# Kernel tuning notes

Hardware: AMD Instinct MI355X
Metric: run time of the kernel (lower is better)

Reference implementation:

```python
import jax, jax.numpy as jnp
import numpy as np

NUM_NODES = 100000
NUM_RELS = 50
NUM_BASES = 16
H_DIM = 16
OUT_DIM = 8
NUM_EDGES = 3200000


def setup_inputs() -> dict:
    key = jax.random.key(0)
    ks = jax.random.split(key, 10)
    inp = {
        "edge_src": jax.random.randint(ks[0], (NUM_EDGES,), 0, NUM_NODES, dtype=jnp.int32),
        "edge_dst": jax.random.randint(ks[1], (NUM_EDGES,), 0, NUM_NODES, dtype=jnp.int32),
        "edge_type": jax.random.randint(ks[2], (NUM_EDGES,), 0, NUM_RELS, dtype=jnp.int32),
        "edge_norm": jax.random.uniform(ks[3], (NUM_EDGES,), dtype=jnp.float32),
        "W0": jax.random.normal(ks[4], (NUM_BASES, NUM_NODES, H_DIM), dtype=jnp.float32) * 0.05,
        "C0": jax.random.normal(ks[5], (NUM_RELS, NUM_BASES), dtype=jnp.float32) * 0.05,
        "W1": jax.random.normal(ks[6], (NUM_BASES, H_DIM, H_DIM), dtype=jnp.float32) * 0.05,
        "C1": jax.random.normal(ks[7], (NUM_RELS, NUM_BASES), dtype=jnp.float32) * 0.05,
        "W2": jax.random.normal(ks[8], (NUM_BASES, H_DIM, OUT_DIM), dtype=jnp.float32) * 0.05,
        "C2": jax.random.normal(ks[9], (NUM_RELS, NUM_BASES), dtype=jnp.float32) * 0.05,
    }
    return inp


def _input_layer(src, dst, rel, norm, W0, C0):
    # basis combination: (R, N, h) embedding-per-relation table
    Wfull = jnp.einsum('rb,bnh->rnh', C0, W0)
    emb = Wfull.reshape(NUM_RELS * NUM_NODES, H_DIM)
    # per-edge gather by rel_type * in_feat + src_id, scaled by norm
    msg = emb[rel * NUM_NODES + src] * norm[:, None]
    h = jax.ops.segment_sum(msg, dst, num_segments=NUM_NODES)
    return jax.nn.relu(h)


def _dense_layer(h, src, dst, rel, norm, W, C, out_dim):
    # basis combination: (R, in, out)
    Wr = jnp.einsum('rb,bio->rio', C, W)
    # transform node features once per relation, then gather by (rel, src)
    Hr = jnp.einsum('ni,rio->rno', h, Wr)  # (R, N, out)
    msg = Hr[rel, src] * norm[:, None]     # (E, out)
    return jax.ops.segment_sum(msg, dst, num_segments=NUM_NODES)


def reference(edge_src, edge_dst, edge_type, edge_norm, W0, C0, W1, C1, W2, C2):
    h = _input_layer(edge_src, edge_dst, edge_type, edge_norm, W0, C0)
    h = jax.nn.relu(_dense_layer(h, edge_src, edge_dst, edge_type, edge_norm, W1, C1, H_DIM))
    h = jax.nn.softmax(_dense_layer(h, edge_src, edge_dst, edge_type, edge_norm, W2, C2, OUT_DIM), axis=1)
    return h
```

## Files before the change

kernel.cpp:

```cpp
#include <hip/hip_runtime.h>
#include <cstddef>
#include <cstdint>

#define E_TOTAL 3200000
#define N_NODES 100000
#define N_RELS 50
#define N_BASES 16
#define HD 16
#define OD 8
#define NTHR 256

#define NBKT 196
#define P1B 1024
#define P1C 3125
#define FP8_SCALE 256.0f
#define FP8_INV (1.0f / 256.0f)

typedef unsigned int u32;
typedef __attribute__((ext_vector_type(8))) short s16x8;
typedef __attribute__((ext_vector_type(4))) float f32x4;
typedef __attribute__((ext_vector_type(16))) float f32x16;

__device__ __forceinline__ u32 cvtpk(float x0, float x1) {
    u32 r;
    asm("v_cvt_pk_bf16_f32 %0, %1, %2" : "=v"(r) : "v"(x0), "v"(x1));
    return r;
}
__device__ __forceinline__ ushort bf16r(float x) {
    u32 a = __float_as_uint(x);
    return (ushort)((a + 0x7fffu + ((a >> 16) & 1u)) >> 16);
}
__device__ __forceinline__ s16x8 as_s16x8(uint4 u) {
    union { uint4 u; s16x8 s; } x; x.u = u; return x.s;
}

#if __has_builtin(__builtin_amdgcn_cvt_pk_fp8_f32)
__device__ __forceinline__ u32 pk8x4(float a, float b, float c, float d) {
    int v = __builtin_amdgcn_cvt_pk_fp8_f32(a, b, 0, false);
    v = __builtin_amdgcn_cvt_pk_fp8_f32(c, d, v, true);
    return (u32)v;
}
#else
__device__ __forceinline__ u32 pk8(float v) {
    u32 x = __float_as_uint(v);
    u32 s = (x >> 24) & 0x80u;
    u32 ax = x & 0x7fffffffu;
    int e = (int)(ax >> 23) - 127;
    if (e < -9) return s;
    if (e < -6) {
        u32 m = (u32)rintf(__uint_as_float(ax) * 512.0f);
        if (m == 0) return s;
        if (m >= 8) return s | 0x08u;
        return s | m;
    }
    u32 m = ax & 0x7fffffu;
    u32 keep = m >> 20, rest = m & 0xFFFFFu;
    keep += (rest > 0x80000u) || (rest == 0x80000u && (keep & 1u));
    u32 ee = (u32)(e + 7);
    if (keep == 8u) { keep = 0u; ee += 1u; }
    if (ee > 15u || (ee == 15u && keep == 7u)) return s | 0x7eu;
    return s | (ee << 3) | keep;
}
__device__ __forceinline__ u32 pk8x4(float a, float b, float c, float d) {
    return pk8(a) | (pk8(b) << 8) | (pk8(c) << 16) | (pk8(d) << 24);
}
#endif
#if __has_builtin(__builtin_amdgcn_cvt_f32_fp8)
template <int SEL>
__device__ __forceinline__ float up8(u32 q) { return __builtin_amdgcn_cvt_f32_fp8(q, SEL); }
#else
template <int SEL>
__device__ __forceinline__ float up8(u32 q) {
    u32 b = (q >> (SEL * 8)) & 0xffu;
    u32 em = b & 0x7fu;
    float v = (em >= 8u) ? __uint_as_float((((em >> 3) + 120u) << 23) | ((em & 7u) << 20))
                         : (float)em * (1.0f / 512.0f);
    return (b & 0x80u) ? -v : v;
}
#endif

__global__ __launch_bounds__(NTHR) void k_p1(const int* __restrict__ esrc, const int* __restrict__ edst,
                                             const int* __restrict__ erel, const float* __restrict__ enorm,
                                             uint2* __restrict__ tmp, int* __restrict__ cntK,
                                             int* __restrict__ runstartK,
                                             const float* __restrict__ W1, const float* __restrict__ C1,
                                             const float* __restrict__ W2, const float* __restrict__ C2,
                                             ushort* __restrict__ f1, ushort* __restrict__ f2) {
    __shared__ int lcnt[NBKT];
    __shared__ int sc[NTHR];
    __shared__ int lcur[NBKT];
    __shared__ uint2 stage[P1C];
    int tid = threadIdx.x;
    if (blockIdx.x >= P1B) {
        int idx = (blockIdx.x - P1B) * NTHR + tid;
        if (idx < 25 * 512) {
            int p = idx >> 9, rem = idx & 511, lane = rem >> 3, e = rem & 7;
            int m = lane & 31, kk = ((lane >> 5) << 3) + e;
            int r = 2 * p + (m >> 4), o = m & 15;
            float acc = 0.f;
            #pragma unroll
            for (int b = 0; b < N_BASES; ++b)
                acc = fmaf(C1[r * N_BASES + b], W1[b * 256 + kk * 16 + o], acc);
            f1[idx] = bf16r(acc * FP8_SCALE);
        } else if (idx < 25 * 512 + 13 * 512) {
            int j = idx - 25 * 512;
            int g = j >> 9, rem = j & 511, lane = rem >> 3, e = rem & 7;
            int m = lane & 31, kk = ((lane >> 5) << 3) + e;
            int rl = 4 * g + (m >> 3), o = m & 7;
            float acc = 0.f;
            if (rl < N_RELS) {
                #pragma unroll
                for (int b = 0; b < N_BASES; ++b)
                    acc = fmaf(C2[rl * N_BASES + b], W2[b * 128 + kk * 8 + o], acc);
            }
            f2[j] = bf16r(acc * FP8_SCALE);
        }
        return;
    }
    for (int i = tid; i < NBKT; i += NTHR) lcnt[i] = 0;
    __syncthreads();
    int e0 = blockIdx.x * P1C;
    u32 rx[13], rn[13];
    int rb[13];
    #pragma unroll
    for (int j = 0; j < 13; ++j) {
        int i = tid + j * NTHR;
        rb[j] = -1;
        if (i < P1C) {
            int e = e0 + i;
            int d = edst[e];
            int b = d >> 9;
            rb[j] = b;
            rx[j] = (u32)esrc[e] | ((u32)erel[e] << 17) | ((u32)(d & 511) << 23);
            rn[j] = __float_as_uint(enorm[e]);
            atomicAdd(&lcnt[b], 1);
        }
    }
    __syncthreads();
    int own = (tid < NBKT) ? lcnt[tid] : 0;
    sc[tid] = own;
    __syncthreads();
    #pragma unroll
    for (int off = 1; off < NTHR; off <<= 1) {
        int t = (tid >= off) ? sc[tid - off] : 0;
        __syncthreads();
        sc[tid] += t;
        __syncthreads();
    }
    if (tid < NBKT) lcur[tid] = sc[tid] - own;
    __syncthreads();
    #pragma unroll
    for (int j = 0; j < 13; ++j) {
        if (rb[j] >= 0) {
            int pos = atomicAdd(&lcur[rb[j]], 1);
            stage[pos] = make_uint2(rx[j], rn[j]);
        }
    }
    __syncthreads();
    for (int i = tid; i < P1C; i += NTHR)
        tmp[(size_t)blockIdx.x * P1C + i] = stage[i];
    for (int b = tid; b < NBKT; b += NTHR) {
        int excl = lcur[b] - lcnt[b];
        cntK[blockIdx.x * NBKT + b] = lcnt[b];
        runstartK[blockIdx.x * NBKT + b] = blockIdx.x * P1C + excl;
    }
}

__global__ __launch_bounds__(NTHR) void k_tot(const int* __restrict__ cntK, int* __restrict__ total) {
    int b = blockIdx.x;
    __shared__ int s[NTHR];
    int tid = threadIdx.x;
    int acc = 0;
    for (int k = tid; k < P1B; k += NTHR) acc += cntK[k * NBKT + b];
    s[tid] = acc;
    __syncthreads();
    for (int off = NTHR / 2; off > 0; off >>= 1) {
        if (tid < off) s[tid] += s[tid + off];
        __syncthreads();
    }
    if (tid == 0) total[b] = s[0];
}

__global__ __launch_bounds__(1024) void k_p2(const uint2* __restrict__ tmp, const int* __restrict__ cntK,
                                             const int* __restrict__ runstartK, const int* __restrict__ total,
                                             uint2* __restrict__ rec, int* __restrict__ row_ptr) {
    int b = blockIdx.x;
    int tid = threadIdx.x;
    __shared__ int dcnt[512], dscan[512];
    __shared__ int gbs;
    if (tid < 256) dcnt[tid] = (tid < b && tid < NBKT) ? total[tid] : 0;
    __syncthreads();
    for (int off = 128; off > 0; off >>= 1) {
        if (tid < off) dcnt[tid] += dcnt[tid + off];
        __syncthreads();
    }
    if (tid == 0) gbs = dcnt[0];
    __syncthreads();
    int gbase = gbs;
    if (tid < 512) dcnt[tid] = 0;
    __syncthreads();
    int mycnt = cntK[tid * NBKT + b];
    int myrs = runstartK[tid * NBKT + b];
    for (int i = 0; i < mycnt; ++i)
        atomicAdd(&dcnt[tmp[myrs + i].x >> 23], 1);
    __syncthreads();
    if (tid < 512) dscan[tid] = dcnt[tid];
    __syncthreads();
    for (int off = 1; off < 512; off <<= 1) {
        int v = (tid >= off && tid < 512) ? dscan[tid - off] : 0;
        __syncthreads();
        if (tid < 512) dscan[tid] += v;
        __syncthreads();
    }
    if (tid < 512) {
        int excl = gbase + dscan[tid] - dcnt[tid];
        int d = (b << 9) + tid;
        if (d < N_NODES) row_ptr[d] = excl;
        dscan[tid] = excl;
    }
    if (b == NBKT - 1 && tid == 0) row_ptr[N_NODES] = E_TOTAL;
    __syncthreads();
    for (int i = 0; i < mycnt; ++i) {
        uint2 t = tmp[myrs + i];
        int pos = atomicAdd(&dscan[t.x >> 23], 1);
        rec[pos] = make_uint2(t.x & 0x7FFFFFu, t.y);
    }
}


__global__ __launch_bounds__(NTHR) void k_emb0(const float* __restrict__ W0, const float* __restrict__ C0,
                                               u32* __restrict__ emb) {
    int tid = threadIdx.x;
    int slot0 = (blockIdx.x * NTHR + tid) * 4;
    __shared__ float c[N_RELS * 16];
    for (int i = tid; i < N_RELS * 16; i += NTHR) c[i] = C0[i] * FP8_SCALE;
    bool ok = slot0 < N_NODES * HD;
    float w[4][16];
    if (ok) {
        #pragma unroll
        for (int b = 0; b < 16; ++b) {
            float4 v = *(const float4*)(W0 + (size_t)b * (N_NODES * HD) + slot0);
            w[0][b] = v.x; w[1][b] = v.y; w[2][b] = v.z; w[3][b] = v.w;
        }
    }
    __syncthreads();
    if (!ok) return;
    for (int r = 0; r < N_RELS; ++r) {
        const float* cr = c + r * 16;
        float a0 = 0.f, a1 = 0.f, a2 = 0.f, a3 = 0.f;
        #pragma unroll
        for (int b = 0; b < 16; ++b) {
            float cb = cr[b];
            a0 = fmaf(cb, w[0][b], a0);
            a1 = fmaf(cb, w[1][b], a1);
            a2 = fmaf(cb, w[2][b], a2);
            a3 = fmaf(cb, w[3][b], a3);
        }
        emb[r * (N_NODES * HD / 4) + (slot0 >> 2)] = pk8x4(a0, a1, a2, a3);
    }
}

__global__ __launch_bounds__(NTHR) void k_g16b(const uint2* __restrict__ rec, const int* __restrict__ row_ptr,
                                               const u32* __restrict__ tbl, u32* __restrict__ hb) {
    int lane = threadIdx.x & 63;
    int g = lane >> 2, l = lane & 3;
    int wave = (blockIdx.x * NTHR + threadIdx.x) >> 6;
    int nw = (gridDim.x * NTHR) >> 6;
    for (int d = wave; d < N_NODES; d += nw) {
        int s0 = row_ptr[d], s1 = row_ptr[d + 1];
        float a0 = 0.f, a1 = 0.f, a2 = 0.f, a3 = 0.f;
        for (int j = s0 + g; j < s1; j += 16) {
            uint2 rc = rec[j];
            int src = rc.x & 0x1FFFF;
            int rel = rc.x >> 17;
            float nm = __uint_as_float(rc.y) * FP8_INV;
            u32 q = tbl[((size_t)rel * N_NODES + src) * 4 + l];
            a0 = fmaf(nm, up8<0>(q), a0);
            a1 = fmaf(nm, up8<1>(q), a1);
            a2 = fmaf(nm, up8<2>(q), a2);
            a3 = fmaf(nm, up8<3>(q), a3);
        }
        a0 += __shfl_xor(a0, 4);  a1 += __shfl_xor(a1, 4);  a2 += __shfl_xor(a2, 4);  a3 += __shfl_xor(a3, 4);
        a0 += __shfl_xor(a0, 8);  a1 += __shfl_xor(a1, 8);  a2 += __shfl_xor(a2, 8);  a3 += __shfl_xor(a3, 8);
        a0 += __shfl_xor(a0, 16); a1 += __shfl_xor(a1, 16); a2 += __shfl_xor(a2, 16); a3 += __shfl_xor(a3, 16);
        a0 += __shfl_xor(a0, 32); a1 += __shfl_xor(a1, 32); a2 += __shfl_xor(a2, 32); a3 += __shfl_xor(a3, 32);
        if (lane < 4) {
            uint2 pk = make_uint2(cvtpk(fmaxf(a0, 0.f), fmaxf(a1, 0.f)),
                                  cvtpk(fmaxf(a2, 0.f), fmaxf(a3, 0.f)));
            *(uint2*)(hb + (size_t)d * 8 + l * 2) = pk;
        }
    }
}

__global__ __launch_bounds__(NTHR) void k_e1f(const uint4* __restrict__ wfrag, const uint4* __restrict__ hb,
                                              u32* __restrict__ emb) {
    const f32x16 z16 = {0.f, 0.f, 0.f, 0.f, 0.f, 0.f, 0.f, 0.f,
                        0.f, 0.f, 0.f, 0.f, 0.f, 0.f, 0.f, 0.f};
    int lane = threadIdx.x & 63;
    int w = (blockIdx.x * NTHR + threadIdx.x) >> 6;
    int p = w / 250, c = w % 250;
    if (p >= 25) return;
    s16x8 af = as_s16x8(wfrag[p * 64 + lane]);
    int col = lane & 31, hi = lane >> 5;
    size_t r0b = (size_t)(2 * p) * 400000, r1b = (size_t)(2 * p + 1) * 400000;
    for (int t = c; t < 3125; t += 250) {
        uint4 hq = hb[(size_t)(t * 32 + col) * 2 + hi];
        f32x16 d = __builtin_amdgcn_mfma_f32_32x32x16_bf16(af, as_s16x8(hq), z16, 0, 0, 0);
        u32 A0 = pk8x4(d[0], d[1], d[2], d[3]);
        u32 B0 = pk8x4(d[4], d[5], d[6], d[7]);
        u32 A1 = pk8x4(d[8], d[9], d[10], d[11]);
        u32 B1 = pk8x4(d[12], d[13], d[14], d[15]);
        u32 pA0 = (u32)__shfl_xor((int)A0, 32);
        u32 pB0 = (u32)__shfl_xor((int)B0, 32);
        u32 pA1 = (u32)__shfl_xor((int)A1, 32);
        u32 pB1 = (u32)__shfl_xor((int)B1, 32);
        u32 off = t * 128 + col * 4;
        if (hi == 0) {
            *(uint2*)(emb + r0b + off) = make_uint2(A0, pA0);
            *(uint2*)(emb + r1b + off) = make_uint2(A1, pA1);
        } else {
            *(uint2*)(emb + r0b + off + 2) = make_uint2(pB0, B0);
            *(uint2*)(emb + r1b + off + 2) = make_uint2(pB1, B1);
        }
    }
}

__global__ __launch_bounds__(NTHR) void k_e2f(const uint4* __restrict__ wfrag, const uint4* __restrict__ hb,
                                              u32* __restrict__ emb) {
    const f32x16 z16 = {0.f, 0.f, 0.f, 0.f, 0.f, 0.f, 0.f, 0.f,
                        0.f, 0.f, 0.f, 0.f, 0.f, 0.f, 0.f, 0.f};
    int lane = threadIdx.x & 63;
    int w = (blockIdx.x * NTHR + threadIdx.x) >> 6;
    int g = w / 250, c = w % 250;
    if (g >= 13) return;
    s16x8 af = as_s16x8(wfrag[g * 64 + lane]);
    int col = lane & 31, hi = lane >> 5;
    for (int t = c; t < 3125; t += 250) {
        uint4 hq = hb[(size_t)(t * 32 + col) * 2 + hi];
        f32x16 d = __builtin_amdgcn_mfma_f32_32x32x16_bf16(af, as_s16x8(hq), z16, 0, 0, 0);
        #pragma unroll
        for (int j = 0; j < 4; ++j) {
            int rl = 4 * g + j;
            if (rl >= N_RELS) break;
            u32 wj = pk8x4(d[4 * j], d[4 * j + 1], d[4 * j + 2], d[4 * j + 3]);
            emb[(size_t)rl * 200000 + t * 64 + col * 2 + hi] = wj;
        }
    }
}

__global__ __launch_bounds__(NTHR) void k_g8sm(const uint2* __restrict__ rec, const int* __restrict__ row_ptr,
                                               const u32* __restrict__ tbl, float* __restrict__ out) {
    int lane = threadIdx.x & 63;
    int g = lane >> 1, l = lane & 1;
    int wave = (blockIdx.x * NTHR + threadIdx.x) >> 6;
    int nw = (gridDim.x * NTHR) >> 6;
    for (int d = wave; d < N_NODES; d += nw) {
        int s0 = row_ptr[d], s1 = row_ptr[d + 1];
        float a0 = 0.f, a1 = 0.f, a2 = 0.f, a3 = 0.f;
        for (int j = s0 + g; j < s1; j += 32) {
            uint2 rc = rec[j];
            int src = rc.x & 0x1FFFF;
            int rel = rc.x >> 17;
            float nm = __uint_as_float(rc.y) * FP8_INV;
            u32 q = tbl[((size_t)rel * N_NODES + src) * 2 + l];
            a0 = fmaf(nm, up8<0>(q), a0);
            a1 = fmaf(nm, up8<1>(q), a1);
            a2 = fmaf(nm, up8<2>(q), a2);
            a3 = fmaf(nm, up8<3>(q), a3);
        }
        a0 += __shfl_xor(a0, 2);  a1 += __shfl_xor(a1, 2);  a2 += __shfl_xor(a2, 2);  a3 += __shfl_xor(a3, 2);
        a0 += __shfl_xor(a0, 4);  a1 += __shfl_xor(a1, 4);  a2 += __shfl_xor(a2, 4);  a3 += __shfl_xor(a3, 4);
        a0 += __shfl_xor(a0, 8);  a1 += __shfl_xor(a1, 8);  a2 += __shfl_xor(a2, 8);  a3 += __shfl_xor(a3, 8);
        a0 += __shfl_xor(a0, 16); a1 += __shfl_xor(a1, 16); a2 += __shfl_xor(a2, 16); a3 += __shfl_xor(a3, 16);
        a0 += __shfl_xor(a0, 32); a1 += __shfl_xor(a1, 32); a2 += __shfl_xor(a2, 32); a3 += __shfl_xor(a3, 32);
        float mx = fmaxf(fmaxf(a0, a1), fmaxf(a2, a3));
        mx = fmaxf(mx, __shfl_xor(mx, 1));
        float e0 = __expf(a0 - mx), e1 = __expf(a1 - mx), e2 = __expf(a2 - mx), e3 = __expf(a3 - mx);
        float sm = e0 + e1 + e2 + e3;
        sm += __shfl_xor(sm, 1);
        float inv = 1.0f / sm;
        if (lane < 2)
            *(float4*)(out + (size_t)d * OD + l * 4) = make_float4(e0 * inv, e1 * inv, e2 * inv, e3 * inv);
    }
}

#define NBLK 2560

__device__ __forceinline__ void fma4(float* acc, float c, float4 w) {
    acc[0] = fmaf(c, w.x, acc[0]);
    acc[1] = fmaf(c, w.y, acc[1]);
    acc[2] = fmaf(c, w.z, acc[2]);
    acc[3] = fmaf(c, w.w, acc[3]);
}

__global__ __launch_bounds__(NTHR) void k_wr(const float* __restrict__ W1, const float* __restrict__ C1,
                                             const float* __restrict__ W2, const float* __restrict__ C2,
                                             float* __restrict__ Wr1, float* __restrict__ Wr2) {
    int idx = blockIdx.x * NTHR + threadIdx.x;
    const int n1 = N_RELS * 256;
    if (idx < n1) {
        int r = idx >> 8, io = idx & 255;
        float acc = 0.f;
        #pragma unroll
        for (int b = 0; b < N_BASES; ++b)
            acc = fmaf(C1[r * N_BASES + b], W1[b * 256 + io], acc);
        Wr1[idx] = acc;
    } else if (idx < n1 + N_RELS * 128) {
        int j = idx - n1;
        int r = j >> 7, io = j & 127;
        float acc = 0.f;
        #pragma unroll
        for (int b = 0; b < N_BASES; ++b)
            acc = fmaf(C2[r * N_BASES + b], W2[b * 128 + io], acc);
        Wr2[j] = acc;
    }
}

__global__ __launch_bounds__(NTHR) void k_l0_old(const int* __restrict__ esrc, const int* __restrict__ edst,
                                                 const int* __restrict__ erel, const float* __restrict__ enorm,
                                                 const float* __restrict__ W0, const float* __restrict__ C0,
                                                 float* __restrict__ h0) {
    for (int e = blockIdx.x * NTHR + threadIdx.x; e < E_TOTAL; e += NBLK * NTHR) {
        int s = esrc[e], d = edst[e], r = erel[e];
        float nm = enorm[e];
        const float4* cp = reinterpret_cast<const float4*>(C0 + r * N_BASES);
        float4 c0 = cp[0], c1 = cp[1], c2 = cp[2], c3 = cp[3];
        float coef[16] = {c0.x, c0.y, c0.z, c0.w, c1.x, c1.y, c1.z, c1.w,
                          c2.x, c2.y, c2.z, c2.w, c3.x, c3.y, c3.z, c3.w};
        float acc[16];
        #pragma unroll
        for (int h = 0; h < 16; ++h) acc[h] = 0.f;
        const float* wbase = W0 + (size_t)s * HD;
        #pragma unroll
        for (int b = 0; b < N_BASES; ++b) {
            const float4* wp = reinterpret_cast<const float4*>(wbase + (size_t)b * (N_NODES * HD));
            float cb = coef[b];
            fma4(acc + 0, cb, wp[0]);
            fma4(acc + 4, cb, wp[1]);
            fma4(acc + 8, cb, wp[2]);
            fma4(acc + 12, cb, wp[3]);
        }
        float* outp = h0 + (size_t)d * HD;
        #pragma unroll
        for (int h = 0; h < 16; ++h) atomicAdd(outp + h, nm * acc[h]);
    }
}

__global__ __launch_bounds__(NTHR) void k_l1_old(const int* __restrict__ esrc, const int* __restrict__ edst,
                                                 const int* __restrict__ erel, const float* __restrict__ enorm,
                                                 const float* __restrict__ h0, const float* __restrict__ Wr1,
                                                 float* __restrict__ h1) {
    __shared__ float w[N_RELS * 260];
    for (int i = threadIdx.x; i < N_RELS * 256; i += NTHR) {
        int r = i >> 8, rest = i & 255;
        w[r * 260 + rest] = Wr1[i];
    }
    __syncthreads();
    for (int e = blockIdx.x * NTHR + threadIdx.x; e < E_TOTAL; e += NBLK * NTHR) {
        int s = esrc[e], d = edst[e], r = erel[e];
        float nm = enorm[e];
        const float4* hp = reinterpret_cast<const float4*>(h0 + (size_t)s * HD);
        float4 hv0 = hp[0], hv1 = hp[1], hv2 = hp[2], hv3 = hp[3];
        float hs[16] = {fmaxf(hv0.x, 0.f), fmaxf(hv0.y, 0.f), fmaxf(hv0.z, 0.f), fmaxf(hv0.w, 0.f),
                        fmaxf(hv1.x, 0.f), fmaxf(hv1.y, 0.f), fmaxf(hv1.z, 0.f), fmaxf(hv1.w, 0.f),
                        fmaxf(hv2.x, 0.f), fmaxf(hv2.y, 0.f), fmaxf(hv2.z, 0.f), fmaxf(hv2.w, 0.f),
                        fmaxf(hv3.x, 0.f), fmaxf(hv3.y, 0.f), fmaxf(hv3.z, 0.f), fmaxf(hv3.w, 0.f)};
        float acc[16];
        #pragma unroll
        for (int h = 0; h < 16; ++h) acc[h] = 0.f;
        const float* wr = w + r * 260;
        #pragma unroll
        for (int i = 0; i < 16; ++i) {
            float hi = hs[i];
            const float4* wp = reinterpret_cast<const float4*>(wr + i * 16);
            fma4(acc + 0, hi, wp[0]);
            fma4(acc + 4, hi, wp[1]);
            fma4(acc + 8, hi, wp[2]);
            fma4(acc + 12, hi, wp[3]);
        }
        float* outp = h1 + (size_t)d * HD;
        #pragma unroll
        for (int h = 0; h < 16; ++h) atomicAdd(outp + h, nm * acc[h]);
    }
}

__global__ __launch_bounds__(NTHR) void k_l2_old(const int* __restrict__ esrc, const int* __restrict__ edst,
                                                 const int* __restrict__ erel, const float* __restrict__ enorm,
                                                 const float* __restrict__ h1, const float* __restrict__ Wr2,
                                                 float* __restrict__ h2) {
    __shared__ float w[N_RELS * 132];
    for (int i = threadIdx.x; i < N_RELS * 128; i += NTHR) {
        int r = i >> 7, rest = i & 127;
        w[r * 132 + rest] = Wr2[i];
    }
    __syncthreads();
    for (int e = blockIdx.x * NTHR + threadIdx.x; e < E_TOTAL; e += NBLK * NTHR) {
        int s = esrc[e], d = edst[e], r = erel[e];
        float nm = enorm[e];
        const float4* hp = reinterpret_cast<const float4*>(h1 + (size_t)s * HD);
        float4 hv0 = hp[0], hv1 = hp[1], hv2 = hp[2], hv3 = hp[3];
        float hs[16] = {fmaxf(hv0.x, 0.f), fmaxf(hv0.y, 0.f), fmaxf(hv0.z, 0.f), fmaxf(hv0.w, 0.f),
                        fmaxf(hv1.x, 0.f), fmaxf(hv1.y, 0.f), fmaxf(hv1.z, 0.f), fmaxf(hv1.w, 0.f),
                        fmaxf(hv2.x, 0.f), fmaxf(hv2.y, 0.f), fmaxf(hv2.z, 0.f), fmaxf(hv2.w, 0.f),
                        fmaxf(hv3.x, 0.f), fmaxf(hv3.y, 0.f), fmaxf(hv3.z, 0.f), fmaxf(hv3.w, 0.f)};
        float acc[8];
        #pragma unroll
        for (int h = 0; h < 8; ++h) acc[h] = 0.f;
        const float* wr = w + r * 132;
        #pragma unroll
        for (int i = 0; i < 16; ++i) {
            float hi = hs[i];
            const float4* wp = reinterpret_cast<const float4*>(wr + i * 8);
            fma4(acc + 0, hi, wp[0]);
            fma4(acc + 4, hi, wp[1]);
        }
        float* outp = h2 + (size_t)d * OD;
        #pragma unroll
        for (int h = 0; h < 8; ++h) atomicAdd(outp + h, nm * acc[h]);
    }
}

__global__ __launch_bounds__(NTHR) void k_softmax(const float* __restrict__ h2, float* __restrict__ out) {
    int n = blockIdx.x * NTHR + threadIdx.x;
    if (n >= N_NODES) return;
    const float4* p = reinterpret_cast<const float4*>(h2 + (size_t)n * OD);
    float4 a = p[0], b = p[1];
    float v[8] = {a.x, a.y, a.z, a.w, b.x, b.y, b.z, b.w};
    float m = v[0];
    #pragma unroll
    for (int i = 1; i < 8; ++i) m = fmaxf(m, v[i]);
    float ssum = 0.f;
    #pragma unroll
    for (int i = 0; i < 8; ++i) {
        v[i] = __expf(v[i] - m);
        ssum += v[i];
    }
    float inv = 1.0f / ssum;
    float4* q = reinterpret_cast<float4*>(out + (size_t)n * OD);
    q[0] = make_float4(v[0] * inv, v[1] * inv, v[2] * inv, v[3] * inv);
    q[1] = make_float4(v[4] * inv, v[5] * inv, v[6] * inv, v[7] * inv);
}


extern "C" void kernel_launch(void* const* d_in, const int* in_sizes, int n_in,
                              void* d_out, int out_size, void* d_ws, size_t ws_size,
                              hipStream_t stream) {
    const int* esrc = (const int*)d_in[0];
    const int* edst = (const int*)d_in[1];
    const int* erel = (const int*)d_in[2];
    const float* enorm = (const float*)d_in[3];
    const float* W0 = (const float*)d_in[4];
    const float* C0 = (const float*)d_in[5];
    const float* W1 = (const float*)d_in[6];
    const float* C1 = (const float*)d_in[7];
    const float* W2 = (const float*)d_in[8];
    const float* C2 = (const float*)d_in[9];
    const int nsb = (N_NODES + NTHR - 1) / NTHR;

    if (ws_size >= (size_t)201000000) {
        char* wsb = (char*)d_ws;
        u32* emb = (u32*)wsb;
        uint2* tmp = (uint2*)wsb;
        uint2* rec = (uint2*)(wsb + 160000000);
        u32* h0b = (u32*)(wsb + 185600000);
        u32* h1b = (u32*)(wsb + 188800000);
        ushort* wf1 = (ushort*)(wsb + 192000000);
        ushort* wf2 = (ushort*)(wsb + 192051200);
        int* row_ptr = (int*)(wsb + 192102400);
        int* cntK = (int*)(wsb + 192502404);
        int* runstartK = (int*)(wsb + 193305220);
        int* total = (int*)(wsb + 194108036);

        k_p1<<<P1B + 76, NTHR, 0, stream>>>(esrc, edst, erel, enorm, tmp, cntK, runstartK,
                                            W1, C1, W2, C2, wf1, wf2);
        k_tot<<<NBKT, NTHR, 0, stream>>>(cntK, total);
        k_p2<<<NBKT, 1024, 0, stream>>>(tmp, cntK, runstartK, total, rec, row_ptr);

        k_emb0<<<1563, NTHR, 0, stream>>>(W0, C0, emb);
        k_g16b<<<6250, NTHR, 0, stream>>>(rec, row_ptr, emb, h0b);
        k_e1f<<<1563, NTHR, 0, stream>>>((const uint4*)wf1, (const uint4*)h0b, emb);
        k_g16b<<<6250, NTHR, 0, stream>>>(rec, row_ptr, emb, h1b);
        k_e2f<<<813, NTHR, 0, stream>>>((const uint4*)wf2, (const uint4*)h1b, emb);
        k_g8sm<<<6250, NTHR, 0, stream>>>(rec, row_ptr, emb, (float*)d_out);
    } else {
        float* ws = (float*)d_ws;
        float* h0 = ws;
        float* h1 = ws + 1600000;
        float* h2 = ws + 3200000;
        float* Wr1 = ws + 4000000;
        float* Wr2 = ws + 4012800;

        (void)hipMemsetAsync(h0, 0, (size_t)4000000 * sizeof(float), stream);
        k_wr<<<75, NTHR, 0, stream>>>(W1, C1, W2, C2, Wr1, Wr2);
        k_l0_old<<<NBLK, NTHR, 0, stream>>>(esrc, edst, erel, enorm, W0, C0, h0);
        k_l1_old<<<NBLK, NTHR, 0, stream>>>(esrc, edst, erel, enorm, h0, Wr1, h1);
        k_l2_old<<<NBLK, NTHR, 0, stream>>>(esrc, edst, erel, enorm, h1, Wr2, h2);
        k_softmax<<<nsb, NTHR, 0, stream>>>(h2, (float*)d_out);
    }
}
```

Baseline: 355.6 us.

## Compute layer-0 relation embeddings with bf16 MFMA in node-major layout

Replaces the scalar FMA basis-combination kernel for layer 0 with a kernel that converts W0 and C0 to bf16 and uses 32x32x16 MFMA to produce all 50 relation embeddings per node chunk. The output table is now laid out node-major (src*200 + rel*4), so the first gather reads the relation rows for a source node from a contiguous region. The gather kernel takes stride parameters so the second layer keeps the old relation-major layout. The trade-off is bf16 rounding of the inputs before the FP8 output, and W0 loads that are now strided scalar reads instead of float4.

```diff
diff --git a/kernel.cpp b/kernel.cpp
--- a/kernel.cpp
+++ b/kernel.cpp
@@ -228,40 +228,52 @@
 }
 
 
-__global__ __launch_bounds__(NTHR) void k_emb0(const float* __restrict__ W0, const float* __restrict__ C0,
-                                               u32* __restrict__ emb) {
-    int tid = threadIdx.x;
-    int slot0 = (blockIdx.x * NTHR + tid) * 4;
-    __shared__ float c[N_RELS * 16];
-    for (int i = tid; i < N_RELS * 16; i += NTHR) c[i] = C0[i] * FP8_SCALE;
-    bool ok = slot0 < N_NODES * HD;
-    float w[4][16];
-    if (ok) {
-        #pragma unroll
-        for (int b = 0; b < 16; ++b) {
-            float4 v = *(const float4*)(W0 + (size_t)b * (N_NODES * HD) + slot0);
-            w[0][b] = v.x; w[1][b] = v.y; w[2][b] = v.z; w[3][b] = v.w;
-        }
-    }
-    __syncthreads();
-    if (!ok) return;
-    for (int r = 0; r < N_RELS; ++r) {
-        const float* cr = c + r * 16;
-        float a0 = 0.f, a1 = 0.f, a2 = 0.f, a3 = 0.f;
-        #pragma unroll
-        for (int b = 0; b < 16; ++b) {
-            float cb = cr[b];
-            a0 = fmaf(cb, w[0][b], a0);
-            a1 = fmaf(cb, w[1][b], a1);
-            a2 = fmaf(cb, w[2][b], a2);
-            a3 = fmaf(cb, w[3][b], a3);
-        }
-        emb[r * (N_NODES * HD / 4) + (slot0 >> 2)] = pk8x4(a0, a1, a2, a3);
+__global__ __launch_bounds__(NTHR) void k_e0f(const float* __restrict__ W0, const float* __restrict__ C0,
+                                              u32* __restrict__ emb) {
+    const f32x16 z16 = {0.f, 0.f, 0.f, 0.f, 0.f, 0.f, 0.f, 0.f,
+                        0.f, 0.f, 0.f, 0.f, 0.f, 0.f, 0.f, 0.f};
+    int lane = threadIdx.x & 63;
+    int col = lane & 31, hi = lane >> 5;
+    s16x8 bf0, bf1;
+    {
+        float v[8];
+        #pragma unroll
+        for (int e = 0; e < 8; ++e) v[e] = C0[col * 16 + hi * 8 + e] * FP8_SCALE;
+        bf0 = as_s16x8(make_uint4(cvtpk(v[0], v[1]), cvtpk(v[2], v[3]),
+                                  cvtpk(v[4], v[5]), cvtpk(v[6], v[7])));
+        int r1 = col + 32;
+        #pragma unroll
+        for (int e = 0; e < 8; ++e) v[e] = (r1 < N_RELS) ? C0[r1 * 16 + hi * 8 + e] * FP8_SCALE : 0.f;
+        bf1 = as_s16x8(make_uint4(cvtpk(v[0], v[1]), cvtpk(v[2], v[3]),
+                                  cvtpk(v[4], v[5]), cvtpk(v[6], v[7])));
+    }
+    int w = (blockIdx.x * NTHR + threadIdx.x) >> 6;
+    int nw = (gridDim.x * NTHR) >> 6;
+    bool g1ok = (col + 32) < N_RELS;
+    for (int t = w; t < 50000; t += nw) {
+        size_t gs = (size_t)t * 32 + col;
+        float a[8];
+        #pragma unroll
+        for (int e = 0; e < 8; ++e)
+            a[e] = W0[(size_t)(hi * 8 + e) * (N_NODES * HD) + gs];
+        s16x8 af = as_s16x8(make_uint4(cvtpk(a[0], a[1]), cvtpk(a[2], a[3]),
+                                       cvtpk(a[4], a[5]), cvtpk(a[6], a[7])));
+        f32x16 d0 = __builtin_amdgcn_mfma_f32_32x32x16_bf16(af, bf0, z16, 0, 0, 0);
+        f32x16 d1 = __builtin_amdgcn_mfma_f32_32x32x16_bf16(af, bf1, z16, 0, 0, 0);
+        #pragma unroll
+        for (int j = 0; j < 4; ++j) {
+            size_t base = ((size_t)(t * 2 + (j >> 1)) * 50) * 4 + (size_t)((j & 1) * 2 + hi);
+            emb[base + (size_t)col * 4] = pk8x4(d0[4 * j], d0[4 * j + 1], d0[4 * j + 2], d0[4 * j + 3]);
+            if (g1ok)
+                emb[base + (size_t)(col + 32) * 4] =
+                    pk8x4(d1[4 * j], d1[4 * j + 1], d1[4 * j + 2], d1[4 * j + 3]);
+        }
     }
 }
 
 __global__ __launch_bounds__(NTHR) void k_g16b(const uint2* __restrict__ rec, const int* __restrict__ row_ptr,
-                                               const u32* __restrict__ tbl, u32* __restrict__ hb) {
+                                               const u32* __restrict__ tbl, u32* __restrict__ hb,
+                                               int srcMul, int relMul) {
     int lane = threadIdx.x & 63;
     int g = lane >> 2, l = lane & 3;
     int wave = (blockIdx.x * NTHR + threadIdx.x) >> 6;
@@ -274,7 +286,7 @@
             int src = rc.x & 0x1FFFF;
             int rel = rc.x >> 17;
             float nm = __uint_as_float(rc.y) * FP8_INV;
-            u32 q = tbl[((size_t)rel * N_NODES + src) * 4 + l];
+            u32 q = tbl[(size_t)src * srcMul + (size_t)rel * relMul + l];
             a0 = fmaf(nm, up8<0>(q), a0);
             a1 = fmaf(nm, up8<1>(q), a1);
             a2 = fmaf(nm, up8<2>(q), a2);
@@ -576,10 +588,10 @@
         k_tot<<<NBKT, NTHR, 0, stream>>>(cntK, total);
         k_p2<<<NBKT, 1024, 0, stream>>>(tmp, cntK, runstartK, total, rec, row_ptr);
 
-        k_emb0<<<1563, NTHR, 0, stream>>>(W0, C0, emb);
-        k_g16b<<<6250, NTHR, 0, stream>>>(rec, row_ptr, emb, h0b);
+        k_e0f<<<1563, NTHR, 0, stream>>>(W0, C0, emb);
+        k_g16b<<<6250, NTHR, 0, stream>>>(rec, row_ptr, emb, h0b, 200, 4);
         k_e1f<<<1563, NTHR, 0, stream>>>((const uint4*)wf1, (const uint4*)h0b, emb);
-        k_g16b<<<6250, NTHR, 0, stream>>>(rec, row_ptr, emb, h1b);
+        k_g16b<<<6250, NTHR, 0, stream>>>(rec, row_ptr, emb, h1b, 4, 400000);
         k_e2f<<<813, NTHR, 0, stream>>>((const uint4*)wf2, (const uint4*)h1b, emb);
         k_g8sm<<<6250, NTHR, 0, stream>>>(rec, row_ptr, emb, (float*)d_out);
     } else {
```

After: 353.5 us. About the same (-0.6%).
